# Kernel optimization log

Measured on AMD Instinct MI355X. Metric: run time of the kernel, lower is better.

## Reference

```python
import jax, jax.numpy as jnp
import numpy as np

IN_CH, HID_CH, OUT_CH, NUM_REL = 128, 256, 128, 8
N_NODES, N_EDGES = 50000, 800000


def _glorot(key, shape):
    fan_in, fan_out = shape[-2], shape[-1]
    lim = float(np.sqrt(6.0 / (fan_in + fan_out)))
    return jax.random.uniform(key, shape, jnp.float32, -lim, lim)


def setup_inputs() -> dict:
    key = jax.random.key(0)
    ks = jax.random.split(key, 12)
    x = jax.random.normal(ks[0], (N_NODES, IN_CH), jnp.float32)
    edge_index = jax.random.randint(ks[1], (2, N_EDGES), 0, N_NODES, jnp.int32)
    edge_type = jax.random.randint(ks[2], (N_EDGES,), 0, NUM_REL, jnp.int32)
    return {
        "x": x, "edge_index": edge_index, "edge_type": edge_type,
        "W1": _glorot(ks[3], (NUM_REL, IN_CH, HID_CH)),
        "root1": _glorot(ks[4], (IN_CH, HID_CH)),
        "b1": jnp.zeros((HID_CH,), jnp.float32),
        "W2": _glorot(ks[5], (NUM_REL, HID_CH, HID_CH)),
        "root2": _glorot(ks[6], (HID_CH, HID_CH)),
        "b2": jnp.zeros((HID_CH,), jnp.float32),
        "W3": _glorot(ks[7], (NUM_REL, HID_CH, OUT_CH)),
        "root3": _glorot(ks[8], (HID_CH, OUT_CH)),
        "b3": jnp.zeros((OUT_CH,), jnp.float32),
    }


def _rgcn_conv(x, src, dst, etype, W, root, b):
    # PyG RGCNConv: per-relation mean aggregation of neighbor features,
    # per-relation linear transform, plus root weight and bias.
    # Linear commutes with mean, so aggregate raw x[src] per (dst, relation)
    # then contract with W: sum_r mean_agg[:, r] @ W[r].
    n, d = x.shape
    r = W.shape[0]
    seg = dst.astype(jnp.int32) * r + etype.astype(jnp.int32)  # [E]
    msg = x[src]                                               # [E, d] gather
    agg = jax.ops.segment_sum(msg, seg, num_segments=n * r)    # [N*R, d]
    cnt = jax.ops.segment_sum(jnp.ones((msg.shape[0],), x.dtype), seg,
                              num_segments=n * r)              # [N*R]
    mean = agg / jnp.maximum(cnt, 1.0)[:, None]                # [N*R, d]
    mean = mean.reshape(n, r, d)
    out = jnp.einsum('nrd,rdo->no', mean, W) + x @ root + b
    return out


def reference(x, edge_index, edge_type, W1, root1, b1, W2, root2, b2, W3, root3, b3):
    src, dst = edge_index[0], edge_index[1]
    h = jax.nn.relu(_rgcn_conv(x, src, dst, edge_type, W1, root1, b1))
    # dropout is identity in eval mode
    h = jax.nn.relu(_rgcn_conv(h, src, dst, edge_type, W2, root2, b2))
    out = _rgcn_conv(h, src, dst, edge_type, W3, root3, b3)
    return out
```

## Files before the change

kernel.cpp:

```cpp
#include <hip/hip_runtime.h>

#define NREL 8
#define SCHUNK 2048

typedef __attribute__((ext_vector_type(8))) short bf16x8;
typedef __attribute__((ext_vector_type(4))) float f32x4;

__device__ __forceinline__ float bf2f(ushort u) {
  union { unsigned u; float f; } c; c.u = ((unsigned)u) << 16; return c.f;
}
__device__ __forceinline__ ushort f2bf(float f) {
  union { float f; unsigned u; } c; c.f = f;
  unsigned r = c.u + 0x7FFFu + ((c.u >> 16) & 1u);
  return (ushort)(r >> 16);
}

__global__ void hist_k(const int* __restrict__ dst, const int* __restrict__ et,
                       int* __restrict__ cnt, int nE) {
  int i = blockIdx.x * blockDim.x + threadIdx.x;
  if (i < nE) atomicAdd(&cnt[dst[i] * NREL + et[i]], 1);
}

__global__ void scan1_k(const int* __restrict__ cnt, int n,
                        int* __restrict__ thexc, int* __restrict__ bsum) {
  __shared__ int sh[256];
  int b = blockIdx.x, t = threadIdx.x;
  int base = b * SCHUNK + t * 8;
  int s = 0;
#pragma unroll
  for (int j = 0; j < 8; ++j) { int idx = base + j; s += (idx < n) ? cnt[idx] : 0; }
  sh[t] = s;
  __syncthreads();
  for (int d = 1; d < 256; d <<= 1) {
    int v = (t >= d) ? sh[t - d] : 0;
    __syncthreads();
    sh[t] += v;
    __syncthreads();
  }
  thexc[b * 256 + t] = sh[t] - s;
  if (t == 255) bsum[b] = sh[255];
}

__global__ void scan2_k(int* __restrict__ bsum, int nb, int total,
                        int* __restrict__ off, int n) {
  int run = 0;
  for (int i = 0; i < nb; ++i) { int v = bsum[i]; bsum[i] = run; run += v; }
  off[n] = total;
}

__global__ void scan3_k(const int* __restrict__ cnt, int n, const int* __restrict__ thexc,
                        const int* __restrict__ bsum, int* __restrict__ off,
                        int* __restrict__ cur) {
  int b = blockIdx.x, t = threadIdx.x;
  int base = b * SCHUNK + t * 8;
  int run = bsum[b] + thexc[b * 256 + t];
#pragma unroll
  for (int j = 0; j < 8; ++j) {
    int idx = base + j;
    if (idx < n) { int c = cnt[idx]; off[idx] = run; cur[idx] = run; run += c; }
  }
}

__global__ void fill2_k(const int* __restrict__ src, const int* __restrict__ dst,
                        const int* __restrict__ et, int nE,
                        int* __restrict__ cur, int* __restrict__ slist) {
  int i = blockIdx.x * blockDim.x + threadIdx.x;
  if (i < nE) {
    int seg = dst[i] * NREL + et[i];
    int p = atomicAdd(&cur[seg], 1);
    slist[p] = src[i];
  }
}

__global__ void f2b_k(const float* __restrict__ in, ushort* __restrict__ out, int n4) {
  int i = blockIdx.x * blockDim.x + threadIdx.x;
  if (i < n4) {
    float4 v = *(const float4*)(in + (size_t)i * 4);
    ushort4 o;
    o.x = f2bf(v.x); o.y = f2bf(v.y); o.z = f2bf(v.z); o.w = f2bf(v.w);
    *(ushort4*)(out + (size_t)i * 4) = o;
  }
}

__global__ void wt_k(const float* __restrict__ W, ushort* __restrict__ Wt,
                     int R, int K, int O, int G) {
  size_t i = (size_t)blockIdx.x * blockDim.x + threadIdx.x;
  size_t tot = (size_t)R * K * O;
  if (i >= tot) return;
  int o = (int)(i % O);
  size_t t = i / O;
  int d = (int)(t % K);
  int r = (int)(t / K);
  Wt[((size_t)(r / G) * O + o) * ((size_t)G * K) + (size_t)(r % G) * K + d] = f2bf(W[i]);
}

template<int D, int NR>
__global__ void gatherN_k(const ushort* __restrict__ xb, const int* __restrict__ slist,
                          const int* __restrict__ off, int r0,
                          ushort* __restrict__ agg, int N) {
  constexpr int V = D / 64;
  int lane = threadIdx.x & 63;
  int d = (blockIdx.x * blockDim.x + threadIdx.x) >> 6;
  if (d >= N) return;
  int o[NR + 1];
#pragma unroll
  for (int j = 0; j <= NR; ++j) o[j] = off[d * NREL + r0 + j];
  const int bc = lane * V;
#pragma unroll
  for (int r = 0; r < NR; ++r) {
    float s[V];
#pragma unroll
    for (int j = 0; j < V; ++j) s[j] = 0.f;
    for (int i = o[r]; i < o[r + 1]; ++i) {
      const ushort* xp = xb + (size_t)slist[i] * D + bc;
      if constexpr (V == 2) {
        uint v = *(const uint*)xp;
        s[0] += bf2f((ushort)(v & 0xffff));
        s[1] += bf2f((ushort)(v >> 16));
      } else {
        ushort4 v = *(const ushort4*)xp;
        s[0] += bf2f(v.x); s[1] += bf2f(v.y); s[2] += bf2f(v.z); s[3] += bf2f(v.w);
      }
    }
    int c = o[r + 1] - o[r];
    float w = 1.f / (float)(c > 1 ? c : 1);
    ushort* mp = agg + (size_t)d * (NR * D) + r * D + bc;
    if constexpr (V == 2) {
      ushort2 st; st.x = f2bf(s[0] * w); st.y = f2bf(s[1] * w);
      *(ushort2*)mp = st;
    } else {
      ushort4 st; st.x = f2bf(s[0] * w); st.y = f2bf(s[1] * w);
      st.z = f2bf(s[2] * w); st.w = f2bf(s[3] * w);
      *(ushort4*)mp = st;
    }
  }
}

template<bool CF32>
__global__ __launch_bounds__(256)
void mgemm_k(const ushort* __restrict__ A, int K, const ushort* __restrict__ Bt,
             const float* __restrict__ bias, void* __restrict__ Cv,
             int loadC, int relu, int M, int O) {
  __shared__ ushort Al[128 * 64];
  __shared__ ushort Bl[128 * 64];
  const int tid = threadIdx.x;
  const int lane = tid & 63;
  const int w = tid >> 6;
  const int wr = (w >> 1) * 64;
  const int wc = (w & 1) * 64;
  const int m0 = blockIdx.x * 128;
  const int n0 = blockIdx.y * 128;

  f32x4 acc[4][4];
#pragma unroll
  for (int i = 0; i < 4; ++i)
#pragma unroll
    for (int j = 0; j < 4; ++j) acc[i][j] = (f32x4){0.f, 0.f, 0.f, 0.f};

  const int srow = tid >> 3;
  const int schk = tid & 7;

  for (int k0 = 0; k0 < K; k0 += 64) {
    __syncthreads();
#pragma unroll
    for (int p = 0; p < 4; ++p) {
      int row = p * 32 + srow;
      int gm = m0 + row;
      uint4 v = make_uint4(0, 0, 0, 0);
      if (gm < M) v = *(const uint4*)(A + (size_t)gm * K + k0 + schk * 8);
      *(uint4*)&Al[row * 64 + ((schk ^ (row & 7)) * 8)] = v;
    }
#pragma unroll
    for (int p = 0; p < 4; ++p) {
      int row = p * 32 + srow;
      uint4 v = *(const uint4*)(Bt + (size_t)(n0 + row) * K + k0 + schk * 8);
      *(uint4*)&Bl[row * 64 + ((schk ^ (row & 7)) * 8)] = v;
    }
    __syncthreads();
#pragma unroll
    for (int kk = 0; kk < 2; ++kk) {
      bf16x8 a_f[4], b_f[4];
      int slot = kk * 4 + (lane >> 4);
#pragma unroll
      for (int f = 0; f < 4; ++f) {
        int mr = wr + f * 16 + (lane & 15);
        a_f[f] = *(const bf16x8*)&Al[mr * 64 + ((slot ^ (mr & 7)) * 8)];
        int nc = wc + f * 16 + (lane & 15);
        b_f[f] = *(const bf16x8*)&Bl[nc * 64 + ((slot ^ (nc & 7)) * 8)];
      }
#pragma unroll
      for (int i = 0; i < 4; ++i)
#pragma unroll
        for (int j = 0; j < 4; ++j)
          acc[i][j] = __builtin_amdgcn_mfma_f32_16x16x32_bf16(a_f[i], b_f[j], acc[i][j], 0, 0, 0);
    }
  }

  float bv[4];
#pragma unroll
  for (int j = 0; j < 4; ++j) bv[j] = bias ? bias[n0 + wc + j * 16 + (lane & 15)] : 0.f;
#pragma unroll
  for (int i = 0; i < 4; ++i) {
#pragma unroll
    for (int rg = 0; rg < 4; ++rg) {
      int row = m0 + wr + i * 16 + (lane >> 4) * 4 + rg;
      if (row < M) {
#pragma unroll
        for (int j = 0; j < 4; ++j) {
          int col = n0 + wc + j * 16 + (lane & 15);
          float v = acc[i][j][rg] + bv[j];
          if (CF32) {
            float* C = (float*)Cv + (size_t)row * O + col;
            if (loadC) v += *C;
            if (relu) v = fmaxf(v, 0.f);
            *C = v;
          } else {
            ushort* C = (ushort*)Cv + (size_t)row * O + col;
            if (loadC) v += bf2f(*C);
            if (relu) v = fmaxf(v, 0.f);
            *C = f2bf(v);
          }
        }
      }
    }
  }
}

extern "C" void kernel_launch(void* const* d_in, const int* in_sizes, int n_in,
                              void* d_out, int out_size, void* d_ws, size_t ws_size,
                              hipStream_t stream) {
  const float* x  = (const float*)d_in[0];
  const int* eidx = (const int*)d_in[1];
  const int* etyp = (const int*)d_in[2];
  const float* W1 = (const float*)d_in[3];
  const float* r1 = (const float*)d_in[4];
  const float* b1 = (const float*)d_in[5];
  const float* W2 = (const float*)d_in[6];
  const float* r2 = (const float*)d_in[7];
  const float* b2 = (const float*)d_in[8];
  const float* W3 = (const float*)d_in[9];
  const float* r3 = (const float*)d_in[10];
  const float* b3 = (const float*)d_in[11];
  float* out = (float*)d_out;

  const int N = in_sizes[0] / 128;
  const int E = in_sizes[2];
  const int* src = eidx;
  const int* dst = eidx + E;
  const int NSEG = N * NREL;
  const int NB = (NSEG + SCHUNK - 1) / SCHUNK;
  (void)n_in; (void)out_size;

  auto al = [](size_t v) { return (v + 255) & ~(size_t)255; };
  char* p = (char*)d_ws;
  int* cnt    = (int*)p;    p += al((size_t)NSEG * 4);
  int* off    = (int*)p;    p += al((size_t)(NSEG + 1) * 4);
  int* thexc  = (int*)p;    p += al((size_t)NB * 256 * 4);
  int* bsum   = (int*)p;    p += al((size_t)NB * 4);
  int* slist  = (int*)p;    p += al((size_t)E * 4);
  ushort* xb  = (ushort*)p; p += al((size_t)N * 128 * 2);
  ushort* h1  = (ushort*)p; p += al((size_t)N * 256 * 2);
  ushort* h2  = (ushort*)p; p += al((size_t)N * 256 * 2);
  ushort* agg = (ushort*)p; p += al((size_t)N * 512 * 2);
  ushort* wt1 = (ushort*)p; p += al((size_t)NREL * 128 * 256 * 2);
  ushort* rt1 = (ushort*)p; p += al((size_t)128 * 256 * 2);
  ushort* wt2 = (ushort*)p; p += al((size_t)NREL * 256 * 256 * 2);
  ushort* rt2 = (ushort*)p; p += al((size_t)256 * 256 * 2);
  ushort* wt3 = (ushort*)p; p += al((size_t)NREL * 256 * 128 * 2);
  ushort* rt3 = (ushort*)p; p += al((size_t)256 * 128 * 2);
  size_t used = (size_t)(p - (char*)d_ws);
  if (used > ws_size) return;

  hipMemsetAsync(d_ws, 0, used, stream);

  hist_k<<<(E + 255) / 256, 256, 0, stream>>>(dst, etyp, cnt, E);
  scan1_k<<<NB, 256, 0, stream>>>(cnt, NSEG, thexc, bsum);
  scan2_k<<<1, 1, 0, stream>>>(bsum, NB, E, off, NSEG);
  scan3_k<<<NB, 256, 0, stream>>>(cnt, NSEG, thexc, bsum, off, cnt);
  fill2_k<<<(E + 255) / 256, 256, 0, stream>>>(src, dst, etyp, E, cnt, slist);

  f2b_k<<<(N * 128 / 4 + 255) / 256, 256, 0, stream>>>(x, xb, N * 128 / 4);
  auto wconv = [&](const float* W, ushort* Wt, int R, int K, int O, int G) {
    size_t tot = (size_t)R * K * O;
    wt_k<<<(int)((tot + 255) / 256), 256, 0, stream>>>(W, Wt, R, K, O, G);
  };
  wconv(W1, wt1, NREL, 128, 256, 4);
  wconv(r1, rt1, 1, 128, 256, 1);
  wconv(W2, wt2, NREL, 256, 256, 2);
  wconv(r2, rt2, 1, 256, 256, 1);
  wconv(W3, wt3, NREL, 256, 128, 2);
  wconv(r3, rt3, 1, 256, 128, 1);

  const int gblocks = (N * 64 + 255) / 256;

  auto layer = [&](const ushort* xin, int D, int NP, const ushort* Wt, const ushort* Rt,
                   const float* bias, void* Y, int O, bool relu, bool cf32) {
    dim3 g((N + 127) / 128, O / 128);
    if (cf32)
      mgemm_k<true><<<g, 256, 0, stream>>>(xin, D, Rt, bias, Y, 0, 0, N, O);
    else
      mgemm_k<false><<<g, 256, 0, stream>>>(xin, D, Rt, bias, Y, 0, 0, N, O);
    int NR = NREL / NP;
    for (int pass = 0; pass < NP; ++pass) {
      if (D == 128)
        gatherN_k<128, 4><<<gblocks, 256, 0, stream>>>(xin, slist, off, pass * 4, agg, N);
      else
        gatherN_k<256, 2><<<gblocks, 256, 0, stream>>>(xin, slist, off, pass * 2, agg, N);
      const ushort* Bt = Wt + (size_t)pass * O * (NR * D);
      int rl = (relu && pass == NP - 1) ? 1 : 0;
      if (cf32)
        mgemm_k<true><<<g, 256, 0, stream>>>(agg, NR * D, Bt, nullptr, Y, 1, rl, N, O);
      else
        mgemm_k<false><<<g, 256, 0, stream>>>(agg, NR * D, Bt, nullptr, Y, 1, rl, N, O);
    }
  };

  layer(xb, 128, 2, wt1, rt1, b1, h1, 256, true,  false);
  layer(h1, 256, 4, wt2, rt2, b2, h2, 256, true,  false);
  layer(h2, 256, 4, wt3, rt3, b3, out, 128, false, true);
}
```

Measured before the change: 1.228 ms.

## Halve gather/GEMM passes, batch gather loads, and prefetch GEMM tiles into registers

Each layer now processes twice as many relations per pass: one pass for layer 1 and two for layers 2 and 3. The aggregation buffer and the weight grouping are doubled to match, which cuts kernel launches and read-modify-write traffic on the fp32/bf16 output. The gather kernel now walks all of a node's edges in one flat loop, issuing four independent row loads before accumulating each into its relation bucket. This is meant to raise memory-level parallelism, at the cost of more registers and per-edge range checks. The GEMM prefetches the next K tile into registers while computing on the current one, adding a second barrier per iteration.

```diff
diff --git a/kernel.cpp b/kernel.cpp
--- a/kernel.cpp
+++ b/kernel.cpp
@@ -99,38 +99,68 @@
                           const int* __restrict__ off, int r0,
                           ushort* __restrict__ agg, int N) {
   constexpr int V = D / 64;
-  int lane = threadIdx.x & 63;
-  int d = (blockIdx.x * blockDim.x + threadIdx.x) >> 6;
+  const int lane = threadIdx.x & 63;
+  const int d = (blockIdx.x * blockDim.x + threadIdx.x) >> 6;
   if (d >= N) return;
   int o[NR + 1];
 #pragma unroll
   for (int j = 0; j <= NR; ++j) o[j] = off[d * NREL + r0 + j];
   const int bc = lane * V;
+  float s[NR][V];
+#pragma unroll
+  for (int r = 0; r < NR; ++r)
+#pragma unroll
+    for (int v = 0; v < V; ++v) s[r][v] = 0.f;
+
+  const int base = o[0], total = o[NR] - base;
+  for (int i0 = 0; i0 < total; i0 += 4) {
+    uint  raw2[4];
+    uint2 raw4[4];
+#pragma unroll
+    for (int u = 0; u < 4; ++u) {
+      if (i0 + u < total) {
+        int e = slist[base + i0 + u];
+        const ushort* xp = xb + (size_t)e * D + bc;
+        if constexpr (V == 2) raw2[u] = *(const uint*)xp;
+        else                  raw4[u] = *(const uint2*)xp;
+      }
+    }
+#pragma unroll
+    for (int u = 0; u < 4; ++u) {
+      if (i0 + u < total) {
+        int gj = base + i0 + u;
+        float f[V];
+        if constexpr (V == 2) {
+          f[0] = bf2f((ushort)(raw2[u] & 0xffff));
+          f[1] = bf2f((ushort)(raw2[u] >> 16));
+        } else {
+          f[0] = bf2f((ushort)(raw4[u].x & 0xffff));
+          f[1] = bf2f((ushort)(raw4[u].x >> 16));
+          f[2] = bf2f((ushort)(raw4[u].y & 0xffff));
+          f[3] = bf2f((ushort)(raw4[u].y >> 16));
+        }
+#pragma unroll
+        for (int r = 0; r < NR; ++r) {
+          if (gj >= o[r] && gj < o[r + 1]) {
+#pragma unroll
+            for (int v = 0; v < V; ++v) s[r][v] += f[v];
+          }
+        }
+      }
+    }
+  }
+
 #pragma unroll
   for (int r = 0; r < NR; ++r) {
-    float s[V];
-#pragma unroll
-    for (int j = 0; j < V; ++j) s[j] = 0.f;
-    for (int i = o[r]; i < o[r + 1]; ++i) {
-      const ushort* xp = xb + (size_t)slist[i] * D + bc;
-      if constexpr (V == 2) {
-        uint v = *(const uint*)xp;
-        s[0] += bf2f((ushort)(v & 0xffff));
-        s[1] += bf2f((ushort)(v >> 16));
-      } else {
-        ushort4 v = *(const ushort4*)xp;
-        s[0] += bf2f(v.x); s[1] += bf2f(v.y); s[2] += bf2f(v.z); s[3] += bf2f(v.w);
-      }
-    }
     int c = o[r + 1] - o[r];
     float w = 1.f / (float)(c > 1 ? c : 1);
     ushort* mp = agg + (size_t)d * (NR * D) + r * D + bc;
     if constexpr (V == 2) {
-      ushort2 st; st.x = f2bf(s[0] * w); st.y = f2bf(s[1] * w);
+      ushort2 st; st.x = f2bf(s[r][0] * w); st.y = f2bf(s[r][1] * w);
       *(ushort2*)mp = st;
     } else {
-      ushort4 st; st.x = f2bf(s[0] * w); st.y = f2bf(s[1] * w);
-      st.z = f2bf(s[2] * w); st.w = f2bf(s[3] * w);
+      ushort4 st; st.x = f2bf(s[r][0] * w); st.y = f2bf(s[r][1] * w);
+      st.z = f2bf(s[r][2] * w); st.w = f2bf(s[r][3] * w);
       *(ushort4*)mp = st;
     }
   }
@@ -160,23 +190,32 @@
   const int srow = tid >> 3;
   const int schk = tid & 7;
 
-  for (int k0 = 0; k0 < K; k0 += 64) {
-    __syncthreads();
+  uint4 ra[4], rb[4];
+  auto gload = [&](int k0) {
 #pragma unroll
     for (int p = 0; p < 4; ++p) {
       int row = p * 32 + srow;
       int gm = m0 + row;
-      uint4 v = make_uint4(0, 0, 0, 0);
-      if (gm < M) v = *(const uint4*)(A + (size_t)gm * K + k0 + schk * 8);
-      *(uint4*)&Al[row * 64 + ((schk ^ (row & 7)) * 8)] = v;
-    }
+      ra[p] = make_uint4(0, 0, 0, 0);
+      if (gm < M) ra[p] = *(const uint4*)(A + (size_t)gm * K + k0 + schk * 8);
+      rb[p] = *(const uint4*)(Bt + (size_t)(n0 + row) * K + k0 + schk * 8);
+    }
+  };
+  auto swrite = [&]() {
 #pragma unroll
     for (int p = 0; p < 4; ++p) {
       int row = p * 32 + srow;
-      uint4 v = *(const uint4*)(Bt + (size_t)(n0 + row) * K + k0 + schk * 8);
-      *(uint4*)&Bl[row * 64 + ((schk ^ (row & 7)) * 8)] = v;
-    }
+      *(uint4*)&Al[row * 64 + ((schk ^ (row & 7)) * 8)] = ra[p];
+      *(uint4*)&Bl[row * 64 + ((schk ^ (row & 7)) * 8)] = rb[p];
+    }
+  };
+
+  gload(0);
+  const int nt = K >> 6;
+  for (int t = 0; t < nt; ++t) {
+    swrite();
     __syncthreads();
+    if (t + 1 < nt) gload((t + 1) << 6);
 #pragma unroll
     for (int kk = 0; kk < 2; ++kk) {
       bf16x8 a_f[4], b_f[4];
@@ -194,6 +233,7 @@
         for (int j = 0; j < 4; ++j)
           acc[i][j] = __builtin_amdgcn_mfma_f32_16x16x32_bf16(a_f[i], b_f[j], acc[i][j], 0, 0, 0);
     }
+    __syncthreads();
   }
 
   float bv[4];
@@ -261,7 +301,7 @@
   ushort* xb  = (ushort*)p; p += al((size_t)N * 128 * 2);
   ushort* h1  = (ushort*)p; p += al((size_t)N * 256 * 2);
   ushort* h2  = (ushort*)p; p += al((size_t)N * 256 * 2);
-  ushort* agg = (ushort*)p; p += al((size_t)N * 512 * 2);
+  ushort* agg = (ushort*)p; p += al((size_t)N * 1024 * 2);
   ushort* wt1 = (ushort*)p; p += al((size_t)NREL * 128 * 256 * 2);
   ushort* rt1 = (ushort*)p; p += al((size_t)128 * 256 * 2);
   ushort* wt2 = (ushort*)p; p += al((size_t)NREL * 256 * 256 * 2);
@@ -284,11 +324,11 @@
     size_t tot = (size_t)R * K * O;
     wt_k<<<(int)((tot + 255) / 256), 256, 0, stream>>>(W, Wt, R, K, O, G);
   };
-  wconv(W1, wt1, NREL, 128, 256, 4);
+  wconv(W1, wt1, NREL, 128, 256, 8);
   wconv(r1, rt1, 1, 128, 256, 1);
-  wconv(W2, wt2, NREL, 256, 256, 2);
+  wconv(W2, wt2, NREL, 256, 256, 4);
   wconv(r2, rt2, 1, 256, 256, 1);
-  wconv(W3, wt3, NREL, 256, 128, 2);
+  wconv(W3, wt3, NREL, 256, 128, 4);
   wconv(r3, rt3, 1, 256, 128, 1);
 
   const int gblocks = (N * 64 + 255) / 256;
@@ -303,9 +343,9 @@
     int NR = NREL / NP;
     for (int pass = 0; pass < NP; ++pass) {
       if (D == 128)
-        gatherN_k<128, 4><<<gblocks, 256, 0, stream>>>(xin, slist, off, pass * 4, agg, N);
+        gatherN_k<128, 8><<<gblocks, 256, 0, stream>>>(xin, slist, off, pass * 8, agg, N);
       else
-        gatherN_k<256, 2><<<gblocks, 256, 0, stream>>>(xin, slist, off, pass * 2, agg, N);
+        gatherN_k<256, 4><<<gblocks, 256, 0, stream>>>(xin, slist, off, pass * 4, agg, N);
       const ushort* Bt = Wt + (size_t)pass * O * (NR * D);
       int rl = (relu && pass == NP - 1) ? 1 : 0;
       if (cf32)
@@ -315,7 +355,7 @@
     }
   };
 
-  layer(xb, 128, 2, wt1, rt1, b1, h1, 256, true,  false);
-  layer(h1, 256, 4, wt2, rt2, b2, h2, 256, true,  false);
-  layer(h2, 256, 4, wt3, rt3, b3, out, 128, false, true);
-}
+  layer(xb, 128, 1, wt1, rt1, b1, h1, 256, true,  false);
+  layer(h1, 256, 2, wt2, rt2, b2, h2, 256, true,  false);
+  layer(h2, 256, 2, wt3, rt3, b3, out, 128, false, true);
+}
```

Measured after the change: 1.186 ms. 1.04x faster.
